# Kernel tuning notes

Hardware: AMD Instinct MI355X
Metric: run time of the kernel (lower is better)

The kernel has to match this reference:

```python
import jax, jax.numpy as jnp
import numpy as np


def setup_inputs() -> dict:
    key = jax.random.key(0)
    k1, = jax.random.split(key, 1)
    B, L, D = 128, 1024, 768
    hidden_states = jax.random.normal(k1, (B, L, D), dtype=jnp.float32)
    attention_mask = jnp.zeros((B, 1, 1, L), dtype=jnp.float32)
    return {"hidden_states": hidden_states, "attention_mask": attention_mask, "K": 512}


def reference(hidden_states, attention_mask, K):
    B, L, D = hidden_states.shape
    # r tokens to merge, protected class token (ToMe: r = min(r, (t - protected)//2))
    r = max(0, L - K)
    r = min(r, (L - 1) // 2)

    # --- bipartite soft matching (indices computed under no_grad in torch) ---
    metric = hidden_states / jnp.linalg.norm(hidden_states, axis=-1, keepdims=True)
    a = metric[:, ::2, :]   # [B, t1, D] even tokens (src side)
    b = metric[:, 1::2, :]  # [B, t2, D] odd tokens (dst side)
    scores = jnp.einsum('bid,bjd->bij', a, b)  # [B, t1, t2]
    scores = scores.at[:, 0, :].set(-jnp.inf)  # protect class token (row 0 of src)
    node_max = jnp.max(scores, axis=-1)        # [B, t1]
    node_idx = jnp.argmax(scores, axis=-1)     # [B, t1] best dst per src
    order = jnp.argsort(-node_max, axis=-1)    # descending similarity
    src_idx = order[:, :r]                     # [B, r] tokens to merge away
    unm_idx = jnp.sort(order[:, r:], axis=-1)  # [B, t1-r] kept src tokens (sorted: class_token=True)
    dst_idx = jnp.take_along_axis(node_idx, src_idx, axis=-1)  # [B, r]

    # --- merge(x, mode='mean') with include_self=True ---
    src = hidden_states[:, ::2, :]   # [B, t1, D]
    dst = hidden_states[:, 1::2, :]  # [B, t2, D]
    t2 = dst.shape[1]
    unm = jnp.take_along_axis(src, unm_idx[..., None], axis=1)     # [B, t1-r, D]
    src_g = jnp.take_along_axis(src, src_idx[..., None], axis=1)   # [B, r, D]
    bidx = jnp.arange(B)[:, None]
    dst_sum = dst.at[bidx, dst_idx].add(src_g)                     # self + merged srcs
    counts = jnp.ones((B, t2), dtype=hidden_states.dtype).at[bidx, dst_idx].add(1.0)
    dst_mean = dst_sum / counts[..., None]

    preserved_tokens = jnp.concatenate([unm, dst_mean], axis=1)    # [B, t1-r+t2, D]
    final_attention_mask = jnp.zeros((B, 1, 1, preserved_tokens.shape[1]),
                                     dtype=hidden_states.dtype)
    return preserved_tokens, final_attention_mask
```

## Files before the change

### kernel.cpp

```cpp
#include <hip/hip_runtime.h>
#include <hip/hip_bf16.h>

#define B_ 128
#define L_ 1024
#define T_ 512
#define D_ 768
#define CH_ 96
#define DT_ 513
#define TAU_C 1e-3f
#define PBUF_ 1024

#define KS_B_CSTR 8208
#define KS_B_BYTES (4 * KS_B_CSTR)
#define KS_A_CSTR 1040
#define KS_A_BYTES (4 * KS_A_CSTR)
#define KS_BYTES (KS_B_BYTES + KS_A_BYTES)
#define SMEM_BYTES (2 * KS_BYTES)

typedef __attribute__((ext_vector_type(8))) short bf16x8;
typedef __attribute__((ext_vector_type(4))) float f32x4;

typedef const __attribute__((address_space(1))) unsigned int* gas1_t;
typedef __attribute__((address_space(3))) unsigned int* gas3_t;

__device__ __forceinline__ unsigned short f2bf_rne(float x){
    unsigned u = __float_as_uint(x);
    unsigned r = (u + 0x7FFFu + ((u >> 16) & 1u)) >> 16;
    return (unsigned short)r;
}

__global__ __launch_bounds__(256) void pack_k(const float* __restrict__ hs,
                                              unsigned short* __restrict__ Apk,
                                              unsigned short* __restrict__ Bpk,
                                              double* __restrict__ nsq,
                                              int* __restrict__ paircnt){
    __shared__ __align__(16) unsigned short LhS[CH_ * 16 * 8];
    if (blockIdx.x == 0 && threadIdx.x == 0) *paircnt = 0;
    int b = blockIdx.x >> 6, g = blockIdx.x & 63;
    int wv = threadIdx.x >> 6, lane = threadIdx.x & 63;

    #pragma unroll
    for (int rr = 0; rr < 4; ++rr){
        int jj = wv * 4 + rr;
        long seq = (long)b * L_ + g * 16 + jj;
        const float4* src = (const float4*)(hs + seq * D_);
        float4 f0 = src[lane], f1 = src[lane + 64], f2 = src[lane + 128];
        double s = 0.0;
        s += (double)f0.x*f0.x + (double)f0.y*f0.y + (double)f0.z*f0.z + (double)f0.w*f0.w;
        s += (double)f1.x*f1.x + (double)f1.y*f1.y + (double)f1.z*f1.z + (double)f1.w*f1.w;
        s += (double)f2.x*f2.x + (double)f2.y*f2.y + (double)f2.z*f2.z + (double)f2.w*f2.w;
        #pragma unroll
        for (int off = 32; off; off >>= 1) s += __shfl_xor(s, off);
        if (lane == 0 && (jj & 1)) nsq[seq] = s;
        float rn = (float)(1.0 / sqrt(s));
        float4 fv[3] = {f0, f1, f2};
        #pragma unroll
        for (int t = 0; t < 3; ++t){
            int e0 = t * 256 + lane * 4;
            int c = e0 >> 3, ei = e0 & 7;
            float vv[4] = {fv[t].x, fv[t].y, fv[t].z, fv[t].w};
            short4 hv;
            #pragma unroll
            for (int e = 0; e < 4; ++e)
                ((short*)&hv)[e] = (short)f2bf_rne(vv[e] * rn);
            int o = c * 128 + ((jj ^ (c & 7)) << 3) + ei;
            *(short4*)(LhS + o) = hv;
        }
    }
    __syncthreads();
    #pragma unroll
    for (int it = 0; it < 6; ++it){
        int linear = it * 256 + threadIdx.x;
        int c = linear >> 4, jj = linear & 15;
        int o = c * 128 + ((jj ^ (c & 7)) << 3);
        int tok = g * 8 + (jj >> 1);
        long go = ((long)(b * CH_ + c) * T_ + tok) * 8;
        if (jj & 1) *(bf16x8*)(Bpk + go) = *(const bf16x8*)(LhS + o);
        else        *(bf16x8*)(Apk + go) = *(const bf16x8*)(LhS + o);
    }
}

__global__ __launch_bounds__(512, 4) void coarse_k(const unsigned short* __restrict__ Apk,
                                                   const unsigned short* __restrict__ Bpk,
                                                   int* __restrict__ node_idx,
                                                   unsigned long long* __restrict__ rowkey,
                                                   int* __restrict__ paircnt,
                                                   int2* __restrict__ pairs){
    __shared__ __align__(16) char SMEM[SMEM_BYTES];

    int bid = blockIdx.x;
    int xcd = bid & 7, q = bid >> 3;
    int it = q & 7, bhi = q >> 3;
    int b = xcd + 8 * bhi;

    int tid = threadIdx.x;
    int w = tid >> 6, lane = tid & 63, l15 = lane & 15, l4 = lane >> 4;

    long pkbase = (long)b * CH_ * T_;

    #define STAGE(s_, slot_) do {                                                          \
        char* dst_ = SMEM + (slot_) * KS_BYTES;                                            \
        _Pragma("unroll")                                                                  \
        for (int n_ = 0; n_ < 4; ++n_){                                                    \
            const unsigned short* sp_ = Bpk + (pkbase + (long)((s_)*4 + n_) * T_ + w * 64 + lane) * 8; \
            __builtin_amdgcn_global_load_lds((gas1_t)sp_, (gas3_t)(dst_ + n_ * KS_B_CSTR + w * 1024), 16, 0, 0); \
        }                                                                                  \
        if (w < 4){                                                                        \
            const unsigned short* sp_ = Apk + (pkbase + (long)((s_)*4 + w) * T_ + it * 64 + lane) * 8; \
            __builtin_amdgcn_global_load_lds((gas1_t)sp_, (gas3_t)(dst_ + KS_B_BYTES + w * KS_A_CSTR), 16, 0, 0); \
        }                                                                                  \
    } while (0)

    f32x4 acc[4][4];
    #pragma unroll
    for (int i = 0; i < 4; ++i)
        #pragma unroll
        for (int j = 0; j < 4; ++j) acc[i][j] = (f32x4){0.f, 0.f, 0.f, 0.f};

    STAGE(0, 0);
    __syncthreads();

    #pragma unroll 2
    for (int s = 0; s < 24; ++s){
        if (s < 23) STAGE(s + 1, (s + 1) & 1);
        const char* slot = SMEM + (s & 1) * KS_BYTES;
        bf16x8 ah[4], bh[4];
        #pragma unroll
        for (int ib = 0; ib < 4; ++ib)
            ah[ib] = *(const bf16x8*)(slot + KS_B_BYTES + l4 * KS_A_CSTR + (ib * 16 + l15) * 16);
        #pragma unroll
        for (int jb = 0; jb < 4; ++jb)
            bh[jb] = *(const bf16x8*)(slot + l4 * KS_B_CSTR + (w * 64 + jb * 16 + l15) * 16);
        __builtin_amdgcn_s_setprio(1);
        #pragma unroll
        for (int jb = 0; jb < 4; ++jb)
            #pragma unroll
            for (int ib = 0; ib < 4; ++ib)
                acc[ib][jb] = __builtin_amdgcn_mfma_f32_16x16x32_bf16(ah[ib], bh[jb], acc[ib][jb], 0, 0, 0);
        __builtin_amdgcn_s_setprio(0);
        asm volatile("s_waitcnt vmcnt(0)" ::: "memory");
        __builtin_amdgcn_s_barrier();
        asm volatile("" ::: "memory");
    }
    #undef STAGE

    float* pm1s = (float*)SMEM;
    int*   pjs  = (int*)(SMEM + 2048);
    float* m1f  = (float*)(SMEM + 4096);
    int*   cnd  = (int*)(SMEM + 4352);
    int2*  pbuf = (int2*)(SMEM + 4608);
    int*   pcnt_s  = (int*)(SMEM + 12800);
    int*   pbase_s = (int*)(SMEM + 12804);

    #pragma unroll
    for (int ib = 0; ib < 4; ++ib)
        #pragma unroll
        for (int rr = 0; rr < 4; ++rr){
            float m1 = -1e30f; int j1 = 0;
            #pragma unroll
            for (int jb = 0; jb < 4; ++jb){
                float v = acc[ib][jb][rr];
                int col = w * 64 + jb * 16 + l15;
                if (v > m1){ m1 = v; j1 = col; }
            }
            #pragma unroll
            for (int m = 1; m < 16; m <<= 1){
                float o1 = __shfl_xor(m1, m);
                int   oj = __shfl_xor(j1, m);
                if (o1 > m1 || (o1 == m1 && oj < j1)){ m1 = o1; j1 = oj; }
            }
            if (l15 == 0){
                int row = ib * 16 + l4 * 4 + rr;
                pm1s[row * 8 + w] = m1; pjs[row * 8 + w] = j1;
            }
        }
    __syncthreads();
    int grow0 = b * T_ + it * 64;
    if (tid < 64){
        float M1 = -1e30f; int J1 = 0;
        #pragma unroll
        for (int w2 = 0; w2 < 8; ++w2){
            float a1 = pm1s[tid * 8 + w2]; int aj = pjs[tid * 8 + w2];
            if (a1 > M1 || (a1 == M1 && aj < J1)){ M1 = a1; J1 = aj; }
        }
        node_idx[grow0 + tid] = J1;
        m1f[tid] = M1;
        cnd[tid] = 0;
        rowkey[grow0 + tid] = 0ULL;
        if (tid == 0) *pcnt_s = 0;
    }
    __syncthreads();
    #pragma unroll
    for (int ib = 0; ib < 4; ++ib)
        #pragma unroll
        for (int rr = 0; rr < 4; ++rr){
            int row = ib * 16 + l4 * 4 + rr;
            float thr_ = m1f[row] - TAU_C;
            int hits = 0;
            #pragma unroll
            for (int jb = 0; jb < 4; ++jb) hits += (acc[ib][jb][rr] > thr_) ? 1 : 0;
            #pragma unroll
            for (int m = 1; m < 16; m <<= 1) hits += __shfl_xor(hits, m);
            if (l15 == 0 && hits) atomicAdd(&cnd[row], hits);
        }
    __syncthreads();
    #pragma unroll
    for (int ib = 0; ib < 4; ++ib)
        #pragma unroll
        for (int rr = 0; rr < 4; ++rr){
            int row = ib * 16 + l4 * 4 + rr;
            if (cnd[row] < 2) continue;
            if (it == 0 && row == 0) continue;
            float thr_ = m1f[row] - TAU_C;
            #pragma unroll
            for (int jb = 0; jb < 4; ++jb)
                if (acc[ib][jb][rr] > thr_){
                    int idx = atomicAdd(pcnt_s, 1);
                    int2 pr = make_int2(grow0 + row, w * 64 + jb * 16 + l15);
                    if (idx < PBUF_) pbuf[idx] = pr;
                    else { int p = atomicAdd(paircnt, 1); pairs[p] = pr; }
                }
        }
    __syncthreads();
    if (tid == 0) *pbase_s = atomicAdd(paircnt, min(*pcnt_s, PBUF_));
    __syncthreads();
    int n = min(*pcnt_s, PBUF_);
    for (int k2 = tid; k2 < n; k2 += 512) pairs[*pbase_s + k2] = pbuf[k2];
}

__global__ __launch_bounds__(256) void refine_k(const float* __restrict__ hs,
                                                const double* __restrict__ nsq,
                                                const int* __restrict__ paircnt,
                                                const int2* __restrict__ pairs,
                                                unsigned long long* __restrict__ rowkey){
    int n = *paircnt;
    int w = threadIdx.x >> 6, lane = threadIdx.x & 63;
    for (int p = blockIdx.x * 4 + w; p < n; p += gridDim.x * 4){
        int2 pr = pairs[p];
        int grow = pr.x, j = pr.y;
        int b = grow >> 9, i = grow & 511;
        const float* ar = hs + ((long)b * L_ + 2 * i) * D_;
        const float* br = hs + ((long)b * L_ + 2 * j + 1) * D_;
        double s = 0.0;
        #pragma unroll
        for (int dd = 0; dd < 12; ++dd){
            int d = dd * 64 + lane;
            s += (double)ar[d] * (double)br[d];
        }
        #pragma unroll
        for (int off = 32; off; off >>= 1) s += __shfl_xor(s, off);
        if (lane == 0){
            double sc = s / sqrt(nsq[(long)b * L_ + 2 * j + 1]);
            unsigned long long bits = (unsigned long long)__double_as_longlong(sc);
            unsigned long long key = (bits >> 63) ? ~bits : (bits | 0x8000000000000000ULL);
            key = (key & ~0xFFFFULL) | (unsigned long long)(511 - j);
            atomicMax(&rowkey[grow], key);
        }
    }
}

__global__ __launch_bounds__(512) void csr_k(const int* __restrict__ node_idx,
                                             const unsigned long long* __restrict__ rowkey,
                                             int* __restrict__ goff,
                                             int* __restrict__ glist){
    __shared__ int sidx[512];
    __shared__ int off[513];
    __shared__ int tmp[512];
    __shared__ int cnt[512];
    int b = blockIdx.x, t = threadIdx.x;
    unsigned long long rk = rowkey[b * T_ + t];
    sidx[t] = rk ? (511 - (int)(rk & 0xFFFFULL)) : node_idx[b * T_ + t];
    cnt[t] = 0;
    __syncthreads();
    if (t >= 1) atomicAdd(&cnt[sidx[t]], 1);
    __syncthreads();
    tmp[t] = cnt[t];
    __syncthreads();
    for (int s = 1; s < 512; s <<= 1){
        int v = (t >= s) ? tmp[t - s] : 0;
        __syncthreads();
        tmp[t] += v;
        __syncthreads();
    }
    if (t == 0) off[0] = 0;
    off[t + 1] = tmp[t];
    __syncthreads();
    if (t >= 1){
        int j = sidx[t], r = 0;
        for (int i2 = 1; i2 < t; ++i2) r += (sidx[i2] == j);
        glist[b * T_ + off[j] + r] = t;
    }
    goff[b * 513 + t] = off[t];
    if (t == 0) goff[b * 513 + 512] = off[512];
}

__global__ __launch_bounds__(192) void merge_k(const float* __restrict__ hs,
                                               const int* __restrict__ goff,
                                               const int* __restrict__ glist,
                                               float* __restrict__ out){
    int bid = blockIdx.x;
    int b = bid / DT_, jj = bid - b * DT_;
    long obase4 = ((long)b * DT_ + jj) * (D_ / 4);
    float4* out4 = (float4*)out;
    if (threadIdx.x == 0) out[(long)B_ * DT_ * D_ + b * DT_ + jj] = 0.0f;
    int d = threadIdx.x;
    if (jj == 0){
        const float4* src = (const float4*)(hs + (long)b * L_ * D_);
        out4[obase4 + d] = src[d];
        return;
    }
    int j = jj - 1;
    int o0 = goff[b * 513 + j], o1 = goff[b * 513 + j + 1];
    const float4* dst = (const float4*)(hs + ((long)b * L_ + 2 * j + 1) * D_);
    float4 a = dst[d];
    for (int s = o0; s < o1; ++s){
        int i = glist[b * T_ + s];
        const float4* srow = (const float4*)(hs + ((long)b * L_ + 2 * i) * D_);
        float4 v = srow[d];
        a.x += v.x; a.y += v.y; a.z += v.z; a.w += v.w;
    }
    float rc = 1.0f / (float)(o1 - o0 + 1);
    a.x *= rc; a.y *= rc; a.z *= rc; a.w *= rc;
    out4[obase4 + d] = a;
}

extern "C" void kernel_launch(void* const* d_in, const int* in_sizes, int n_in,
                              void* d_out, int out_size, void* d_ws, size_t ws_size,
                              hipStream_t stream){
    const float* hs = (const float*)d_in[0];
    float* out = (float*)d_out;
    char* ws = (char*)d_ws;

    const long PSZ = (long)B_ * CH_ * T_ * 8;
    unsigned short* Apk = (unsigned short*)ws;
    unsigned short* Bpk = Apk + PSZ;
    double* nsq      = (double*)(ws + 201326592);
    int*    node_idx = (int*)   (ws + 202375168);
    unsigned long long* rowkey = (unsigned long long*)(ws + 202637312);
    int*    paircnt  = (int*)   (ws + 203161600);
    int*    goff     = (int*)   (ws + 203161856);
    int*    glist    = (int*)   (ws + 203425024);
    int2*   pairs    = (int2*)  (ws + 203687168);

    pack_k  <<<B_ * 64, 256, 0, stream>>>(hs, Apk, Bpk, nsq, paircnt);
    coarse_k<<<B_ * 8, 512, 0, stream>>>(Apk, Bpk, node_idx, rowkey, paircnt, pairs);
    refine_k<<<512, 256, 0, stream>>>(hs, nsq, paircnt, pairs, rowkey);
    csr_k   <<<B_, 512, 0, stream>>>(node_idx, rowkey, goff, glist);
    merge_k <<<B_ * DT_, 192, 0, stream>>>(hs, goff, glist, out);
}
```

Measured before the change: 342.0 us.

## Retile coarse GEMM into 128x128 blocks with split-column partial max reduction

The coarse similarity kernel changes from 64 rows × 512 columns per 512-thread block to 128×128 tiles in 256-thread blocks, with a 4-way split over the destination columns. Per-tile top-2 maxima are written out, and a new reduce kernel combines them into node_idx and a per-row ambiguity threshold. Candidate pairs now carry their coarse score, so refine skips pairs that fall below the final threshold. The trade-off: more blocks and a larger reuse-friendly tile, but an extra kernel launch and more conservative pair emission, since the local block max is used. Double buffering of the K-stage loads is also dropped in favour of a simple load/sync loop.

```diff
diff --git a/kernel.cpp b/kernel.cpp
--- a/kernel.cpp
+++ b/kernel.cpp
@@ -9,13 +9,6 @@
 #define DT_ 513
 #define TAU_C 1e-3f
 #define PBUF_ 1024
-
-#define KS_B_CSTR 8208
-#define KS_B_BYTES (4 * KS_B_CSTR)
-#define KS_A_CSTR 1040
-#define KS_A_BYTES (4 * KS_A_CSTR)
-#define KS_BYTES (KS_B_BYTES + KS_A_BYTES)
-#define SMEM_BYTES (2 * KS_BYTES)
 
 typedef __attribute__((ext_vector_type(8))) short bf16x8;
 typedef __attribute__((ext_vector_type(4))) float f32x4;
@@ -80,34 +73,35 @@
     }
 }
 
-__global__ __launch_bounds__(512, 4) void coarse_k(const unsigned short* __restrict__ Apk,
+__global__ __launch_bounds__(256, 3) void coarse_k(const unsigned short* __restrict__ Apk,
                                                    const unsigned short* __restrict__ Bpk,
-                                                   int* __restrict__ node_idx,
-                                                   unsigned long long* __restrict__ rowkey,
+                                                   float* __restrict__ pmax1,
+                                                   float* __restrict__ pmax2,
+                                                   int*   __restrict__ pj1,
                                                    int* __restrict__ paircnt,
-                                                   int2* __restrict__ pairs){
-    __shared__ __align__(16) char SMEM[SMEM_BYTES];
+                                                   int2* __restrict__ pairs_ij,
+                                                   float* __restrict__ pairv){
+    __shared__ __align__(16) char SMEM[32768];
 
     int bid = blockIdx.x;
-    int xcd = bid & 7, q = bid >> 3;
-    int it = q & 7, bhi = q >> 3;
+    int xcd = bid & 7, rest = bid >> 3;
+    int it = rest & 3, jt = (rest >> 2) & 3, bhi = rest >> 4;
     int b = xcd + 8 * bhi;
 
     int tid = threadIdx.x;
     int w = tid >> 6, lane = tid & 63, l15 = lane & 15, l4 = lane >> 4;
+    int wr = w >> 1, wc = w & 1;
 
     long pkbase = (long)b * CH_ * T_;
 
-    #define STAGE(s_, slot_) do {                                                          \
-        char* dst_ = SMEM + (slot_) * KS_BYTES;                                            \
+    #define STG(sk) do {                                                                   \
         _Pragma("unroll")                                                                  \
         for (int n_ = 0; n_ < 4; ++n_){                                                    \
-            const unsigned short* sp_ = Bpk + (pkbase + (long)((s_)*4 + n_) * T_ + w * 64 + lane) * 8; \
-            __builtin_amdgcn_global_load_lds((gas1_t)sp_, (gas3_t)(dst_ + n_ * KS_B_CSTR + w * 1024), 16, 0, 0); \
-        }                                                                                  \
-        if (w < 4){                                                                        \
-            const unsigned short* sp_ = Apk + (pkbase + (long)((s_)*4 + w) * T_ + it * 64 + lane) * 8; \
-            __builtin_amdgcn_global_load_lds((gas1_t)sp_, (gas3_t)(dst_ + KS_B_BYTES + w * KS_A_CSTR), 16, 0, 0); \
+            int seg_ = w * 4 + n_, c_ = seg_ >> 1, h_ = seg_ & 1;                          \
+            const unsigned short* sa_ = Apk + (pkbase + (long)((sk)*8 + c_) * T_ + it * 128 + h_ * 64 + lane) * 8; \
+            __builtin_amdgcn_global_load_lds((gas1_t)sa_, (gas3_t)(SMEM + (c_ * 128 + h_ * 64) * 16), 16, 0, 0);   \
+            const unsigned short* sb_ = Bpk + (pkbase + (long)((sk)*8 + c_) * T_ + jt * 128 + h_ * 64 + lane) * 8; \
+            __builtin_amdgcn_global_load_lds((gas1_t)sb_, (gas3_t)(SMEM + 16384 + (c_ * 128 + h_ * 64) * 16), 16, 0, 0); \
         }                                                                                  \
     } while (0)
 
@@ -117,127 +111,146 @@
         #pragma unroll
         for (int j = 0; j < 4; ++j) acc[i][j] = (f32x4){0.f, 0.f, 0.f, 0.f};
 
-    STAGE(0, 0);
-    __syncthreads();
-
-    #pragma unroll 2
-    for (int s = 0; s < 24; ++s){
-        if (s < 23) STAGE(s + 1, (s + 1) & 1);
-        const char* slot = SMEM + (s & 1) * KS_BYTES;
-        bf16x8 ah[4], bh[4];
-        #pragma unroll
-        for (int ib = 0; ib < 4; ++ib)
-            ah[ib] = *(const bf16x8*)(slot + KS_B_BYTES + l4 * KS_A_CSTR + (ib * 16 + l15) * 16);
-        #pragma unroll
-        for (int jb = 0; jb < 4; ++jb)
-            bh[jb] = *(const bf16x8*)(slot + l4 * KS_B_CSTR + (w * 64 + jb * 16 + l15) * 16);
-        __builtin_amdgcn_s_setprio(1);
-        #pragma unroll
-        for (int jb = 0; jb < 4; ++jb)
+    STG(0);
+    __syncthreads();
+
+    for (int s = 0; s < 12; ++s){
+        #pragma unroll
+        for (int kk = 0; kk < 2; ++kk){
+            bf16x8 ah[4], bh[4];
             #pragma unroll
             for (int ib = 0; ib < 4; ++ib)
-                acc[ib][jb] = __builtin_amdgcn_mfma_f32_16x16x32_bf16(ah[ib], bh[jb], acc[ib][jb], 0, 0, 0);
-        __builtin_amdgcn_s_setprio(0);
-        asm volatile("s_waitcnt vmcnt(0)" ::: "memory");
-        __builtin_amdgcn_s_barrier();
-        asm volatile("" ::: "memory");
-    }
-    #undef STAGE
-
-    float* pm1s = (float*)SMEM;
-    int*   pjs  = (int*)(SMEM + 2048);
-    float* m1f  = (float*)(SMEM + 4096);
-    int*   cnd  = (int*)(SMEM + 4352);
-    int2*  pbuf = (int2*)(SMEM + 4608);
-    int*   pcnt_s  = (int*)(SMEM + 12800);
-    int*   pbase_s = (int*)(SMEM + 12804);
+                ah[ib] = *(const bf16x8*)(SMEM + (((kk*4 + l4) * 128) + wr * 64 + ib * 16 + l15) * 16);
+            #pragma unroll
+            for (int jb = 0; jb < 4; ++jb)
+                bh[jb] = *(const bf16x8*)(SMEM + 16384 + (((kk*4 + l4) * 128) + wc * 64 + jb * 16 + l15) * 16);
+            #pragma unroll
+            for (int jb = 0; jb < 4; ++jb)
+                #pragma unroll
+                for (int ib = 0; ib < 4; ++ib)
+                    acc[ib][jb] = __builtin_amdgcn_mfma_f32_16x16x32_bf16(ah[ib], bh[jb], acc[ib][jb], 0, 0, 0);
+        }
+        __syncthreads();
+        if (s < 11){
+            STG(s + 1);
+            __syncthreads();
+        }
+    }
+    #undef STG
+
+    float* pm1s  = (float*)SMEM;
+    float* pm2s  = (float*)(SMEM + 1024);
+    int*   pjs   = (int*)  (SMEM + 2048);
+    float* m1blk = (float*)(SMEM + 3072);
+    int2*  pb_ij = (int2*) (SMEM + 4096);
+    float* pb_v  = (float*)(SMEM + 12288);
+    int*   pcnt_s  = (int*)(SMEM + 16384);
+    int*   pbase_s = (int*)(SMEM + 16388);
+    if (tid == 0) *pcnt_s = 0;
 
     #pragma unroll
     for (int ib = 0; ib < 4; ++ib)
         #pragma unroll
         for (int rr = 0; rr < 4; ++rr){
-            float m1 = -1e30f; int j1 = 0;
+            float m1 = -1e30f, m2 = -1e30f; int j1 = 0;
             #pragma unroll
             for (int jb = 0; jb < 4; ++jb){
                 float v = acc[ib][jb][rr];
-                int col = w * 64 + jb * 16 + l15;
-                if (v > m1){ m1 = v; j1 = col; }
+                int col = wc * 64 + jb * 16 + l15;
+                if (v > m1){ m2 = m1; m1 = v; j1 = col; }
+                else m2 = fmaxf(m2, v);
             }
             #pragma unroll
             for (int m = 1; m < 16; m <<= 1){
                 float o1 = __shfl_xor(m1, m);
+                float o2 = __shfl_xor(m2, m);
                 int   oj = __shfl_xor(j1, m);
-                if (o1 > m1 || (o1 == m1 && oj < j1)){ m1 = o1; j1 = oj; }
+                if (o1 > m1){ m2 = fmaxf(m1, o2); m1 = o1; j1 = oj; }
+                else if (o1 < m1){ m2 = fmaxf(m2, o1); }
+                else { m2 = m1; j1 = min(j1, oj); }
             }
             if (l15 == 0){
-                int row = ib * 16 + l4 * 4 + rr;
-                pm1s[row * 8 + w] = m1; pjs[row * 8 + w] = j1;
+                int row = wr * 64 + ib * 16 + l4 * 4 + rr;
+                pm1s[row * 2 + wc] = m1; pm2s[row * 2 + wc] = m2; pjs[row * 2 + wc] = j1;
             }
         }
     __syncthreads();
-    int grow0 = b * T_ + it * 64;
-    if (tid < 64){
-        float M1 = -1e30f; int J1 = 0;
-        #pragma unroll
-        for (int w2 = 0; w2 < 8; ++w2){
-            float a1 = pm1s[tid * 8 + w2]; int aj = pjs[tid * 8 + w2];
-            if (a1 > M1 || (a1 == M1 && aj < J1)){ M1 = a1; J1 = aj; }
-        }
-        node_idx[grow0 + tid] = J1;
-        m1f[tid] = M1;
-        cnd[tid] = 0;
-        rowkey[grow0 + tid] = 0ULL;
-        if (tid == 0) *pcnt_s = 0;
+    int grow0 = b * T_ + it * 128;
+    if (tid < 128){
+        float M1 = -1e30f, M2 = -1e30f; int J1 = 0;
+        #pragma unroll
+        for (int c2 = 0; c2 < 2; ++c2){
+            float a1 = pm1s[tid * 2 + c2], a2 = pm2s[tid * 2 + c2]; int aj = pjs[tid * 2 + c2];
+            if (a1 > M1){ M2 = fmaxf(M1, a2); M1 = a1; J1 = aj; }
+            else { M2 = fmaxf(M2, a1); }
+        }
+        long pidx = (long)(grow0 + tid) * 4 + jt;
+        pmax1[pidx] = M1; pmax2[pidx] = M2; pj1[pidx] = jt * 128 + J1;
+        m1blk[tid] = M1;
     }
     __syncthreads();
     #pragma unroll
     for (int ib = 0; ib < 4; ++ib)
         #pragma unroll
         for (int rr = 0; rr < 4; ++rr){
-            int row = ib * 16 + l4 * 4 + rr;
-            float thr_ = m1f[row] - TAU_C;
-            int hits = 0;
-            #pragma unroll
-            for (int jb = 0; jb < 4; ++jb) hits += (acc[ib][jb][rr] > thr_) ? 1 : 0;
-            #pragma unroll
-            for (int m = 1; m < 16; m <<= 1) hits += __shfl_xor(hits, m);
-            if (l15 == 0 && hits) atomicAdd(&cnd[row], hits);
-        }
-    __syncthreads();
-    #pragma unroll
-    for (int ib = 0; ib < 4; ++ib)
-        #pragma unroll
-        for (int rr = 0; rr < 4; ++rr){
-            int row = ib * 16 + l4 * 4 + rr;
-            if (cnd[row] < 2) continue;
+            int row = wr * 64 + ib * 16 + l4 * 4 + rr;
             if (it == 0 && row == 0) continue;
-            float thr_ = m1f[row] - TAU_C;
-            #pragma unroll
-            for (int jb = 0; jb < 4; ++jb)
-                if (acc[ib][jb][rr] > thr_){
+            float thr_ = m1blk[row] - TAU_C;
+            #pragma unroll
+            for (int jb = 0; jb < 4; ++jb){
+                float v = acc[ib][jb][rr];
+                if (v > thr_){
                     int idx = atomicAdd(pcnt_s, 1);
-                    int2 pr = make_int2(grow0 + row, w * 64 + jb * 16 + l15);
-                    if (idx < PBUF_) pbuf[idx] = pr;
-                    else { int p = atomicAdd(paircnt, 1); pairs[p] = pr; }
+                    int2 pr = make_int2(grow0 + row, jt * 128 + wc * 64 + jb * 16 + l15);
+                    if (idx < PBUF_){ pb_ij[idx] = pr; pb_v[idx] = v; }
+                    else { int p = atomicAdd(paircnt, 1); pairs_ij[p] = pr; pairv[p] = v; }
                 }
+            }
         }
     __syncthreads();
     if (tid == 0) *pbase_s = atomicAdd(paircnt, min(*pcnt_s, PBUF_));
     __syncthreads();
     int n = min(*pcnt_s, PBUF_);
-    for (int k2 = tid; k2 < n; k2 += 512) pairs[*pbase_s + k2] = pbuf[k2];
+    for (int k2 = tid; k2 < n; k2 += 256){
+        pairs_ij[*pbase_s + k2] = pb_ij[k2];
+        pairv  [*pbase_s + k2] = pb_v[k2];
+    }
+}
+
+__global__ __launch_bounds__(256) void reduce_k(const float* __restrict__ pmax1,
+                                                const float* __restrict__ pmax2,
+                                                const int*   __restrict__ pj1,
+                                                int* __restrict__ node_idx,
+                                                float* __restrict__ thr,
+                                                unsigned long long* __restrict__ rowkey){
+    int t = blockIdx.x * 256 + threadIdx.x;
+    if (t >= B_ * T_) return;
+    float M1 = -1e30f, M2 = -1e30f; int J1 = 0;
+    #pragma unroll
+    for (int cb = 0; cb < 4; ++cb){
+        float a1 = pmax1[(long)t * 4 + cb], a2 = pmax2[(long)t * 4 + cb];
+        int aj = pj1[(long)t * 4 + cb];
+        if (a1 > M1){ M2 = fmaxf(M1, a2); M1 = a1; J1 = aj; }
+        else { M2 = fmaxf(M2, a1); }
+    }
+    node_idx[t] = J1;
+    thr[t] = ((t & (T_ - 1)) != 0 && (M1 - M2) < TAU_C) ? (M1 - TAU_C) : 3.0e38f;
+    rowkey[t] = 0ULL;
 }
 
 __global__ __launch_bounds__(256) void refine_k(const float* __restrict__ hs,
                                                 const double* __restrict__ nsq,
                                                 const int* __restrict__ paircnt,
-                                                const int2* __restrict__ pairs,
+                                                const int2* __restrict__ pairs_ij,
+                                                const float* __restrict__ pairv,
+                                                const float* __restrict__ thr,
                                                 unsigned long long* __restrict__ rowkey){
     int n = *paircnt;
     int w = threadIdx.x >> 6, lane = threadIdx.x & 63;
     for (int p = blockIdx.x * 4 + w; p < n; p += gridDim.x * 4){
-        int2 pr = pairs[p];
+        int2 pr = pairs_ij[p];
         int grow = pr.x, j = pr.y;
+        if (pairv[p] <= thr[grow]) continue;
         int b = grow >> 9, i = grow & 511;
         const float* ar = hs + ((long)b * L_ + 2 * i) * D_;
         const float* br = hs + ((long)b * L_ + 2 * j + 1) * D_;
@@ -340,11 +353,17 @@
     int*    paircnt  = (int*)   (ws + 203161600);
     int*    goff     = (int*)   (ws + 203161856);
     int*    glist    = (int*)   (ws + 203425024);
-    int2*   pairs    = (int2*)  (ws + 203687168);
+    float*  pmax1    = (float*) (ws + 203687168);
+    float*  pmax2    = (float*) (ws + 204735744);
+    int*    pj1      = (int*)   (ws + 205784320);
+    float*  thr      = (float*) (ws + 206832896);
+    int2*   pairs_ij = (int2*)  (ws + 207095040);
+    float*  pairv    = (float*) (ws + 223872256);
 
     pack_k  <<<B_ * 64, 256, 0, stream>>>(hs, Apk, Bpk, nsq, paircnt);
-    coarse_k<<<B_ * 8, 512, 0, stream>>>(Apk, Bpk, node_idx, rowkey, paircnt, pairs);
-    refine_k<<<512, 256, 0, stream>>>(hs, nsq, paircnt, pairs, rowkey);
+    coarse_k<<<2048, 256, 0, stream>>>(Apk, Bpk, pmax1, pmax2, pj1, paircnt, pairs_ij, pairv);
+    reduce_k<<<B_ * T_ / 256, 256, 0, stream>>>(pmax1, pmax2, pj1, node_idx, thr, rowkey);
+    refine_k<<<512, 256, 0, stream>>>(hs, nsq, paircnt, pairs_ij, pairv, thr, rowkey);
     csr_k   <<<B_, 512, 0, stream>>>(node_idx, rowkey, goff, glist);
     merge_k <<<B_ * DT_, 192, 0, stream>>>(hs, goff, glist, out);
 }
```

Result: slower. 396.9 us (+16.0%).
